# Kernel tuning notes

Measured on AMD Instinct MI355X. Metric: run time of the kernel, lower is better.

Reference implementation:

```python
import jax, jax.numpy as jnp
import numpy as np

EPS = 1e-6
TEMP_GEO = 0.07
W_LOCAL = 0.5
W_SHARP = 0.5


def _l2norm(x):
    return x / jnp.clip(jnp.linalg.norm(x, axis=-1, keepdims=True), 1e-12)


def setup_inputs() -> dict:
    key = jax.random.key(0)
    ks = jax.random.split(key, 6)
    B, L, S, C = 8, 1024, 1024, 128
    N, P = 8, 256
    q_geo = _l2norm(jax.random.normal(ks[0], (B, L, C), jnp.float32))
    geo_pos = _l2norm(jax.random.normal(ks[1], (B, S, C), jnp.float32))
    label = jax.random.randint(ks[2], (B, L, S), 0, 2, jnp.int32)
    q_cl = jax.random.normal(ks[3], (N, P, C), jnp.float32)
    cl_pos = jax.random.normal(ks[4], (N, P, C), jnp.float32)
    idx = jax.random.randint(ks[5], (N,), 0, P, jnp.int32)
    return {"q_geo": q_geo, "q_cl": q_cl, "geo_pos": geo_pos,
            "cl_pos": cl_pos, "label": label, "idx": idx}


def _masked_mean(v, m):
    # per-sample mean over the [L,S] plane of entries where m is True
    m = m.astype(v.dtype)
    return jnp.sum(v * m, axis=(1, 2)) / jnp.maximum(jnp.sum(m, axis=(1, 2)), 1.0)


def _loftr_loss(conf, label):
    # standard LoFTR coarse CE loss (LoFTRLoss source absent from repo snippet)
    conf = jnp.clip(conf, EPS, 1.0 - EPS)
    pos = label == 1
    neg = label == 0
    pos_loss = _masked_mean(-jnp.log(conf), pos)          # [B]
    neg_loss = _masked_mean(-jnp.log(1.0 - conf), neg)    # [B]
    loss = pos_loss + neg_loss
    return jnp.mean(loss), jnp.mean(pos_loss), jnp.mean(neg_loss)


def _geometric_loss(q, k, label):
    sim = jnp.einsum('blc,bsc->bls', q, k) / TEMP_GEO        # [B,L,S]
    conf = jax.nn.softmax(sim, axis=1) * jax.nn.softmax(sim, axis=2)
    return _loftr_loss(conf, label)


def _sharpness_loss(q, k, label):
    sim = (1.0 + jnp.einsum('blc,bsc->bls', q, k)) / 2.0     # [B,L,S]
    # column stats (over L, dim=0 per sample) -> sharpness1 [B,S]
    s1 = (jnp.max(sim, axis=1) - jnp.mean(sim, axis=1)) / jnp.std(sim, axis=1, ddof=1)
    sharp1 = jax.nn.softmax(s1, axis=-1)
    # row stats (over S, dim=1 per sample) -> sharpness2 [B,L]
    s2 = (jnp.max(sim, axis=2) - jnp.mean(sim, axis=2)) / jnp.std(sim, axis=2, ddof=1)
    sharp2 = jax.nn.softmax(s2, axis=-1)
    simc = jnp.clip(sim, EPS, 1.0 - EPS)
    nll = -jnp.log(simc)
    pos = (label == 1).astype(simc.dtype)
    neg = (label == 0)
    loss1 = jnp.sum(nll * sharp1[:, None, :] * pos, axis=(1, 2))   # [B]
    loss2 = jnp.sum(nll * sharp2[:, :, None] * pos, axis=(1, 2))   # [B]
    loss3 = _masked_mean(-jnp.log(1.0 - simc), neg)                # [B]
    losses = (loss1 + loss2) / 2.0 + loss3
    return sharp1, jnp.mean(losses)


def _contrast_loss(q, all_k):
    # intended math of GeCoContrast: full cosine matrix, diag positives, tail negatives
    N = q.shape[0]
    sim = (1.0 + _l2norm(q) @ _l2norm(all_k).T) / 2.0   # [N, M]
    sim = jnp.clip(sim, EPS, 1.0 - EPS)
    l_pos = jnp.diagonal(sim[:, :N])                    # [N]
    l_neg = sim[:, N:]                                  # [N, M-N]
    return (jnp.mean(-jnp.log(l_pos)) + jnp.mean(-jnp.log(1.0 - l_neg))) / 2.0


def _forward(q_geo, q_cl, geo_pos, cl_pos, label, idx):
    loss_geo, geo_pos_loss, geo_neg_loss = _geometric_loss(q_geo, geo_pos, label)
    sharpness, loss_sharp = _sharpness_loss(q_geo, geo_pos, label)
    loss_geo = ((1.0 - W_SHARP) * loss_geo + W_SHARP * loss_sharp) * W_LOCAL

    N, P, C = q_cl.shape
    ar = jnp.arange(N)
    q_sel = q_cl[ar, idx]                               # [N,C]
    sel = cl_pos[ar, idx]                               # [N,C] positives moved to slot 0
    first = cl_pos[:, 0, :]
    swapped = cl_pos.at[ar, idx].set(first).at[:, 0, :].set(sel)
    cl_pos_save = sel
    all_k = jnp.concatenate([swapped[:, 0, :],
                             swapped[:, 1:, :].reshape(N * (P - 1), C)], axis=0)
    loss_cl = _contrast_loss(q_sel, all_k) * (1.0 - W_LOCAL)

    total = loss_geo + loss_cl
    return (sharpness, cl_pos_save, total, geo_pos_loss, geo_neg_loss, loss_sharp, loss_cl)


def reference(q_geo, q_cl, geo_pos, cl_pos, label, idx):
    return _forward(q_geo, q_cl, geo_pos, cl_pos, label, idx)
```

## Files before the change

### kernel.cpp

```cpp
#include <hip/hip_runtime.h>
#include <math.h>

#define BB 8
#define LL 1024
#define SS 1024
#define CC 128
#define NN 8
#define PP 256

static constexpr float EPS       = 1e-6f;
static constexpr float ONE_M_EPS = 1.0f - 1e-6f;
static constexpr float INV_T     = 1.0f / 0.07f;
static constexpr float NLL_MAX   = 13.815511f;
static constexpr float NLL_MIN   = 1.0000005e-6f;

static constexpr size_t DOTSZ      = (size_t)BB * LL * SS;
static constexpr size_t OFF_LSER   = DOTSZ;
static constexpr size_t OFF_LSEC   = DOTSZ + 16384;
static constexpr size_t OFF_SHARP2 = DOTSZ + 32768;
static constexpr size_t OFF_RP     = DOTSZ + 40960;
static constexpr size_t OFF_CP     = OFF_RP + 524288;
static constexpr size_t OFF_ACC    = OFF_CP + 524288;
static constexpr size_t OFF_ACCCL  = OFF_ACC + 48;
static constexpr size_t OFF_QN     = OFF_ACC + 64;

static constexpr int OUT_CLSAVE = 8192;
static constexpr int OUT_SCAL   = 9216;

typedef __bf16 bf16x8 __attribute__((ext_vector_type(8)));
typedef float  floatx4 __attribute__((ext_vector_type(4)));

__device__ __forceinline__ bf16x8 mkfrag(unsigned a, unsigned b, unsigned c, unsigned d) {
    uint4 t = make_uint4(a, b, c, d);
    return __builtin_bit_cast(bf16x8, t);
}

__device__ __forceinline__ void split_f4(float4 x,
                                         unsigned& hp0, unsigned& hp1,
                                         unsigned& lp0, unsigned& lp1) {
    unsigned u0 = __builtin_bit_cast(unsigned, x.x);
    unsigned u1 = __builtin_bit_cast(unsigned, x.y);
    unsigned u2 = __builtin_bit_cast(unsigned, x.z);
    unsigned u3 = __builtin_bit_cast(unsigned, x.w);
    unsigned r0 = u0 + 0x7FFFu + ((u0 >> 16) & 1u);
    unsigned r1 = u1 + 0x7FFFu + ((u1 >> 16) & 1u);
    unsigned r2 = u2 + 0x7FFFu + ((u2 >> 16) & 1u);
    unsigned r3 = u3 + 0x7FFFu + ((u3 >> 16) & 1u);
    float s0 = x.x - __builtin_bit_cast(float, r0 & 0xFFFF0000u);
    float s1 = x.y - __builtin_bit_cast(float, r1 & 0xFFFF0000u);
    float s2 = x.z - __builtin_bit_cast(float, r2 & 0xFFFF0000u);
    float s3 = x.w - __builtin_bit_cast(float, r3 & 0xFFFF0000u);
    hp0 = __builtin_amdgcn_perm(r1, r0, 0x07060302u);
    hp1 = __builtin_amdgcn_perm(r3, r2, 0x07060302u);
    lp0 = __builtin_amdgcn_perm(__builtin_bit_cast(unsigned, s1),
                                __builtin_bit_cast(unsigned, s0), 0x07060302u);
    lp1 = __builtin_amdgcn_perm(__builtin_bit_cast(unsigned, s3),
                                __builtin_bit_cast(unsigned, s2), 0x07060302u);
}

__global__ __launch_bounds__(256) void gemm_dot(const float* __restrict__ A,
                                                const float* __restrict__ Bm,
                                                const float* __restrict__ q_cl,
                                                const float* __restrict__ cl_pos,
                                                const int* __restrict__ idx,
                                                float* __restrict__ out,
                                                float* __restrict__ dot,
                                                float* __restrict__ ws) {
    int tid  = threadIdx.x;
    int lane = tid & 63;
    int w    = tid >> 6;

    if (blockIdx.x == 512) {
        if (tid < 52) ws[OFF_ACC + tid] = 0.0f;
        for (int n = w; n < NN; n += 4) {
            int in = idx[n];
            const float* q = q_cl + ((size_t)(n * PP + in)) * CC;
            float2 qv = *(const float2*)(q + 2 * lane);
            float ss = qv.x * qv.x + qv.y * qv.y;
            for (int o = 32; o; o >>= 1) ss += __shfl_xor(ss, o);
            float inv = 1.0f / fmaxf(sqrtf(ss), 1e-12f);
            *(float2*)(ws + OFF_QN + n * 128 + 2 * lane) = make_float2(qv.x * inv, qv.y * inv);
            const float* cp = cl_pos + ((size_t)(n * PP + in)) * CC;
            float2 cv = *(const float2*)(cp + 2 * lane);
            *(float2*)(out + OUT_CLSAVE + n * 128 + 2 * lane) = cv;
        }
        return;
    }

    int t    = blockIdx.x * 4 + w;
    int b    = t >> 8;
    int rem  = t & 255;
    int lt   = rem >> 4, st = rem & 15;
    int l0   = lt * 64, s0 = st * 64;
    int fl   = lane & 15;
    int quad = lane >> 4;

    const float* Ab = A  + ((size_t)b * LL + l0) * CC;
    const float* Bb = Bm + ((size_t)b * SS + s0) * CC;

    floatx4 acc[4][4];
#pragma unroll
    for (int i = 0; i < 4; i++)
#pragma unroll
        for (int j = 0; j < 4; j++) acc[i][j] = (floatx4){0.f, 0.f, 0.f, 0.f};

    for (int c0 = 0; c0 < 128; c0 += 32) {
        float4 ax[4][2], bx[4][2];
#pragma unroll
        for (int mt = 0; mt < 4; mt++) {
            const float* p = Ab + (size_t)(mt * 16 + fl) * CC + c0 + quad * 8;
            ax[mt][0] = *(const float4*)p;
            ax[mt][1] = *(const float4*)(p + 4);
        }
#pragma unroll
        for (int nt = 0; nt < 4; nt++) {
            const float* p = Bb + (size_t)(nt * 16 + fl) * CC + c0 + quad * 8;
            bx[nt][0] = *(const float4*)p;
            bx[nt][1] = *(const float4*)(p + 4);
        }
        bf16x8 ah[4], al[4];
#pragma unroll
        for (int mt = 0; mt < 4; mt++) {
            unsigned h0, h1, h2, h3, q0, q1, q2, q3;
            split_f4(ax[mt][0], h0, h1, q0, q1);
            split_f4(ax[mt][1], h2, h3, q2, q3);
            ah[mt] = mkfrag(h0, h1, h2, h3);
            al[mt] = mkfrag(q0, q1, q2, q3);
        }
#pragma unroll
        for (int nt = 0; nt < 4; nt++) {
            unsigned h0, h1, h2, h3, q0, q1, q2, q3;
            split_f4(bx[nt][0], h0, h1, q0, q1);
            split_f4(bx[nt][1], h2, h3, q2, q3);
            bf16x8 bh = mkfrag(h0, h1, h2, h3);
            bf16x8 bl = mkfrag(q0, q1, q2, q3);
#pragma unroll
            for (int mt = 0; mt < 4; mt++) {
                acc[mt][nt] = __builtin_amdgcn_mfma_f32_16x16x32_bf16(ah[mt], bh, acc[mt][nt], 0, 0, 0);
                acc[mt][nt] = __builtin_amdgcn_mfma_f32_16x16x32_bf16(ah[mt], bl, acc[mt][nt], 0, 0, 0);
                acc[mt][nt] = __builtin_amdgcn_mfma_f32_16x16x32_bf16(al[mt], bh, acc[mt][nt], 0, 0, 0);
            }
        }
    }

    float* D = dot + ((size_t)b * LL + l0) * SS + s0;
#pragma unroll
    for (int mt = 0; mt < 4; mt++)
#pragma unroll
        for (int nt = 0; nt < 4; nt++) {
            int col = nt * 16 + fl;
#pragma unroll
            for (int r = 0; r < 4; r++) {
                int row = mt * 16 + quad * 4 + r;
                D[(size_t)row * SS + col] = acc[mt][nt][r];
            }
        }

    float ces[4], cmx[4], csm[4], csq[4];
#pragma unroll
    for (int nt = 0; nt < 4; nt++) { ces[nt] = 0.f; cmx[nt] = -1e30f; csm[nt] = 0.f; csq[nt] = 0.f; }
#pragma unroll
    for (int mt = 0; mt < 4; mt++) {
#pragma unroll
        for (int r = 0; r < 4; r++) {
            float es = 0.f, mx = -1e30f, sm = 0.f, sq = 0.f;
#pragma unroll
            for (int nt = 0; nt < 4; nt++) {
                float d  = acc[mt][nt][r];
                float e  = __expf(d * INV_T);
                float s2 = fmaf(0.5f, d, 0.5f);
                es += e; mx = fmaxf(mx, s2); sm += s2; sq += s2 * s2;
                ces[nt] += e; cmx[nt] = fmaxf(cmx[nt], s2); csm[nt] += s2; csq[nt] += s2 * s2;
            }
            for (int o = 1; o < 16; o <<= 1) {
                es += __shfl_xor(es, o);
                mx = fmaxf(mx, __shfl_xor(mx, o));
                sm += __shfl_xor(sm, o);
                sq += __shfl_xor(sq, o);
            }
            if (fl == 0) {
                int row = l0 + mt * 16 + quad * 4 + r;
                *(float4*)(ws + OFF_RP + (((size_t)(b * 16 + st)) * 1024 + row) * 4) =
                    make_float4(es, mx, sm, sq);
            }
        }
    }
#pragma unroll
    for (int nt = 0; nt < 4; nt++) {
        float es = ces[nt], mx = cmx[nt], sm = csm[nt], sq = csq[nt];
        for (int o = 16; o < 64; o <<= 1) {
            es += __shfl_xor(es, o);
            mx = fmaxf(mx, __shfl_xor(mx, o));
            sm += __shfl_xor(sm, o);
            sq += __shfl_xor(sq, o);
        }
        if (quad == 0) {
            int col = s0 + nt * 16 + fl;
            *(float4*)(ws + OFF_CP + (((size_t)(b * 16 + lt)) * 1024 + col) * 4) =
                make_float4(es, mx, sm, sq);
        }
    }
}

__global__ __launch_bounds__(256) void mid(const float* __restrict__ cl_pos,
                                           const int* __restrict__ idx,
                                           float* __restrict__ ws,
                                           float* __restrict__ out) {
    int q   = blockIdx.x;
    int tid = threadIdx.x;
    int lane = tid & 63, wid = tid >> 6;

    if (q < 16) {
        bool docol = (q < 8);
        int b = q & 7;
        const float* part = ws + (docol ? OFF_CP : OFF_RP) + (size_t)b * 16 * 1024 * 4;
        float* lse = ws + (docol ? OFF_LSEC : OFF_LSER) + (size_t)b * 1024;
        float zs[4];
        float mxall = -1e30f;
#pragma unroll
        for (int r = 0; r < 4; r++) {
            int i = tid + r * 256;
            float es = 0.f, mx = -1e30f, sm = 0.f, sq = 0.f;
#pragma unroll
            for (int t = 0; t < 16; t++) {
                float4 v = *(const float4*)(part + ((size_t)t * 1024 + i) * 4);
                es += v.x; mx = fmaxf(mx, v.y); sm += v.z; sq += v.w;
            }
            float mean = sm * (1.0f / 1024.0f);
            float var  = (sq - sm * sm * (1.0f / 1024.0f)) * (1.0f / 1023.0f);
            zs[r] = (mx - mean) / sqrtf(fmaxf(var, 1e-30f));
            mxall = fmaxf(mxall, zs[r]);
            lse[i] = __logf(es);
        }
        __shared__ float sb[4];
        __shared__ float red;
        float mx = mxall;
        for (int o = 32; o; o >>= 1) mx = fmaxf(mx, __shfl_xor(mx, o));
        if (!lane) sb[wid] = mx;
        __syncthreads();
        if (tid == 0) red = fmaxf(fmaxf(sb[0], sb[1]), fmaxf(sb[2], sb[3]));
        __syncthreads();
        mx = red;
        float e[4]; float smv = 0.f;
#pragma unroll
        for (int r = 0; r < 4; r++) { e[r] = __expf(zs[r] - mx); smv += e[r]; }
        for (int o = 32; o; o >>= 1) smv += __shfl_xor(smv, o);
        __syncthreads();
        if (!lane) sb[wid] = smv;
        __syncthreads();
        if (tid == 0) red = sb[0] + sb[1] + sb[2] + sb[3];
        __syncthreads();
        float inv = 1.0f / red;
        float* dst = docol ? (out + (size_t)b * 1024) : (ws + OFF_SHARP2 + (size_t)b * 1024);
#pragma unroll
        for (int r = 0; r < 4; r++) dst[tid + r * 256] = e[r] * inv;
    } else {
        int j = (q - 16) * 4 + wid;
        int m, p;
        if (j < NN) {
            m = j; p = idx[j];
        } else {
            int jj = j - NN;
            m = jj / (PP - 1);
            p = 1 + (jj - m * (PP - 1));
            if (p == idx[m]) p = 0;
        }
        const float* k = cl_pos + ((size_t)(m * PP + p)) * CC;
        float2 kv = *(const float2*)(k + 2 * lane);
        float ksq = kv.x * kv.x + kv.y * kv.y;
        for (int o = 32; o; o >>= 1) ksq += __shfl_xor(ksq, o);
        float invkn = 1.0f / fmaxf(sqrtf(ksq), 1e-12f);
        float pos = 0.0f, neg = 0.0f;
        if (j < NN) {
            const float2 qv = *(const float2*)(ws + OFF_QN + j * 128 + 2 * lane);
            float dt = qv.x * kv.x + qv.y * kv.y;
            for (int o = 32; o; o >>= 1) dt += __shfl_xor(dt, o);
            float sim = fminf(fmaxf(fmaf(0.5f * invkn, dt, 0.5f), EPS), ONE_M_EPS);
            pos = -__logf(sim);
        } else {
#pragma unroll
            for (int n = 0; n < NN; n++) {
                const float2 qv = *(const float2*)(ws + OFF_QN + n * 128 + 2 * lane);
                float dt = qv.x * kv.x + qv.y * kv.y;
                for (int o = 32; o; o >>= 1) dt += __shfl_xor(dt, o);
                float om = fminf(fmaxf(fmaf(-0.5f * invkn, dt, 0.5f), EPS), ONE_M_EPS);
                neg -= __logf(om);
            }
        }
        __shared__ float cb[2][4];
        if (!lane) { cb[0][wid] = pos; cb[1][wid] = neg; }
        __syncthreads();
        if (tid == 0) {
            float ps = cb[0][0] + cb[0][1] + cb[0][2] + cb[0][3];
            float ng = cb[1][0] + cb[1][1] + cb[1][2] + cb[1][3];
            if (ps != 0.0f) atomicAdd(ws + OFF_ACCCL + 0, ps);
            if (ng != 0.0f) atomicAdd(ws + OFF_ACCCL + 1, ng);
        }
    }
}

__device__ __forceinline__ void proc_elem(float d, int lab, float lcj, float sh1j,
                                          float lr, float s2v,
                                          float& posg, float& negg, float& l1, float& l2,
                                          float& negs, float& pcf) {
    float t = lr + lcj - d * (2.0f * INV_T);
    float isPos = (lab == 1) ? 1.0f : 0.0f;
    float isNeg = 1.0f - isPos;
    float tp   = fminf(fmaxf(t, NLL_MIN), NLL_MAX);
    float simc = fminf(fmaxf(fmaf(0.5f, d, 0.5f), EPS), ONE_M_EPS);
    float om   = fminf(fmaxf(fmaf(-0.5f, d, 0.5f), EPS), ONE_M_EPS);
    float nll2 = -__logf(simc);
    float cf   = fminf(fmaxf(__expf(-t), EPS), ONE_M_EPS);
    float nllg = -__logf(1.0f - cf);
    float nlls = -__logf(om);
    posg += isPos * tp;
    l1   += isPos * nll2 * sh1j;
    l2   += isPos * nll2 * s2v;
    pcf  += isPos;
    negg += isNeg * nllg;
    negs += isNeg * nlls;
}

__global__ __launch_bounds__(256) void main_loss(const float* __restrict__ dot,
                                                 const int* __restrict__ label,
                                                 const float* __restrict__ sharp1,
                                                 float* __restrict__ ws) {
    int b = blockIdx.y;
    int l0 = blockIdx.x * 4;
    int s = threadIdx.x * 4;
    float4 lc4 = *(const float4*)(ws + OFF_LSEC + (size_t)b * 1024 + s);
    float4 sh1 = *(const float4*)(sharp1 + (size_t)b * 1024 + s);
    const float* lser = ws + OFF_LSER + (size_t)b * 1024;
    const float* sh2  = ws + OFF_SHARP2 + (size_t)b * 1024;
    float posg = 0, negg = 0, l1 = 0, l2 = 0, negs = 0, pcf = 0;
#pragma unroll
    for (int r = 0; r < 4; r++) {
        int l = l0 + r;
        float lr  = lser[l];
        float s2v = sh2[l];
        size_t base = ((size_t)(b * 1024 + l)) * 1024 + s;
        float4 d4 = *(const float4*)(dot + base);
        int4  lb  = *(const int4*)(label + base);
        proc_elem(d4.x, lb.x, lc4.x, sh1.x, lr, s2v, posg, negg, l1, l2, negs, pcf);
        proc_elem(d4.y, lb.y, lc4.y, sh1.y, lr, s2v, posg, negg, l1, l2, negs, pcf);
        proc_elem(d4.z, lb.z, lc4.z, sh1.z, lr, s2v, posg, negg, l1, l2, negs, pcf);
        proc_elem(d4.w, lb.w, lc4.w, sh1.w, lr, s2v, posg, negg, l1, l2, negs, pcf);
    }
    float vals[6] = {posg, negg, l1, l2, negs, pcf};
    __shared__ float sb[6][4];
    int lane = threadIdx.x & 63, wid = threadIdx.x >> 6;
#pragma unroll
    for (int k = 0; k < 6; k++) {
        float v = vals[k];
        for (int o = 32; o; o >>= 1) v += __shfl_xor(v, o);
        if (!lane) sb[k][wid] = v;
    }
    __syncthreads();
    if (threadIdx.x < 6) {
        float r = sb[threadIdx.x][0] + sb[threadIdx.x][1] + sb[threadIdx.x][2] + sb[threadIdx.x][3];
        atomicAdd(ws + OFF_ACC + (size_t)b * 6 + threadIdx.x, r);
    }
}

__global__ void finalize(float* __restrict__ out, const float* __restrict__ ws) {
    if (threadIdx.x != 0) return;
    float gp = 0, gn = 0, lsh = 0;
    for (int b = 0; b < 8; b++) {
        const float* a = ws + OFF_ACC + (size_t)b * 6;
        float pc = a[5];
        float nc = (float)((size_t)LL * SS) - pc;
        gp += a[0] / fmaxf(pc, 1.0f);
        gn += a[1] / fmaxf(nc, 1.0f);
        lsh += (a[2] + a[3]) * 0.5f + a[4] / fmaxf(nc, 1.0f);
    }
    gp *= 0.125f; gn *= 0.125f; lsh *= 0.125f;
    float lgeo = gp + gn;
    float lgw = (0.5f * lgeo + 0.5f * lsh) * 0.5f;
    float clp = ws[OFF_ACCCL + 0] / 8.0f;
    float cln = ws[OFF_ACCCL + 1] / (8.0f * 2040.0f);
    float lcl = (clp + cln) * 0.5f * 0.5f;
    out[OUT_SCAL + 0] = lgw + lcl;
    out[OUT_SCAL + 1] = gp;
    out[OUT_SCAL + 2] = gn;
    out[OUT_SCAL + 3] = lsh;
    out[OUT_SCAL + 4] = lcl;
}

extern "C" void kernel_launch(void* const* d_in, const int* in_sizes, int n_in,
                              void* d_out, int out_size, void* d_ws, size_t ws_size,
                              hipStream_t stream) {
    const float* q_geo   = (const float*)d_in[0];
    const float* q_cl    = (const float*)d_in[1];
    const float* geo_pos = (const float*)d_in[2];
    const float* cl_pos  = (const float*)d_in[3];
    const int*   label   = (const int*)d_in[4];
    const int*   idx     = (const int*)d_in[5];
    float* out = (float*)d_out;
    float* ws  = (float*)d_ws;
    float* dot = ws;

    gemm_dot<<<dim3(513), dim3(256), 0, stream>>>(q_geo, geo_pos, q_cl, cl_pos, idx, out, dot, ws);
    mid<<<dim3(528), dim3(256), 0, stream>>>(cl_pos, idx, ws, out);
    main_loss<<<dim3(256, 8), dim3(256), 0, stream>>>(dot, label, out, ws);
    finalize<<<dim3(1), dim3(64), 0, stream>>>(out, ws);
}
```

Measured before the change: 158.9 us.

## Recompute similarity GEMM in loss kernel instead of storing dot matrix

Removes the 32 MB fp32 dot-product buffer. The GEMM now runs twice: once to produce row and column statistics, and again in the loss kernel, which consumes the MFMA accumulators directly together with the labels. Tiles shrink to 32x64 per wave to raise block count and cut register use, so column partials grow to 32 slices. This trades extra MFMA work for avoiding a large global write and re-read. Label loads become strided 16-wide per row instead of float4-vectorized.

Result: slower. 201.4 us (+26.7%).

```diff
diff --git a/kernel.cpp b/kernel.cpp
--- a/kernel.cpp
+++ b/kernel.cpp
@@ -14,13 +14,12 @@
 static constexpr float NLL_MAX   = 13.815511f;
 static constexpr float NLL_MIN   = 1.0000005e-6f;
 
-static constexpr size_t DOTSZ      = (size_t)BB * LL * SS;
-static constexpr size_t OFF_LSER   = DOTSZ;
-static constexpr size_t OFF_LSEC   = DOTSZ + 16384;
-static constexpr size_t OFF_SHARP2 = DOTSZ + 32768;
-static constexpr size_t OFF_RP     = DOTSZ + 40960;
+static constexpr size_t OFF_LSER   = 0;
+static constexpr size_t OFF_LSEC   = 8192;
+static constexpr size_t OFF_SHARP2 = 16384;
+static constexpr size_t OFF_RP     = 24576;
 static constexpr size_t OFF_CP     = OFF_RP + 524288;
-static constexpr size_t OFF_ACC    = OFF_CP + 524288;
+static constexpr size_t OFF_ACC    = OFF_CP + 1048576;
 static constexpr size_t OFF_ACCCL  = OFF_ACC + 48;
 static constexpr size_t OFF_QN     = OFF_ACC + 64;
 
@@ -58,19 +57,66 @@
                                 __builtin_bit_cast(unsigned, s2), 0x07060302u);
 }
 
-__global__ __launch_bounds__(256) void gemm_dot(const float* __restrict__ A,
-                                                const float* __restrict__ Bm,
-                                                const float* __restrict__ q_cl,
-                                                const float* __restrict__ cl_pos,
-                                                const int* __restrict__ idx,
-                                                float* __restrict__ out,
-                                                float* __restrict__ dot,
-                                                float* __restrict__ ws) {
+__device__ __forceinline__ void gemm_tile(const float* __restrict__ Ab,
+                                          const float* __restrict__ Bb,
+                                          int fl, int quad, floatx4 acc[2][4]) {
+#pragma unroll
+    for (int i = 0; i < 2; i++)
+#pragma unroll
+        for (int j = 0; j < 4; j++) acc[i][j] = (floatx4){0.f, 0.f, 0.f, 0.f};
+
+    for (int c0 = 0; c0 < 128; c0 += 32) {
+        float4 ax[2][2], bx[4][2];
+#pragma unroll
+        for (int mt = 0; mt < 2; mt++) {
+            const float* p = Ab + (size_t)(mt * 16 + fl) * CC + c0 + quad * 8;
+            ax[mt][0] = *(const float4*)p;
+            ax[mt][1] = *(const float4*)(p + 4);
+        }
+#pragma unroll
+        for (int nt = 0; nt < 4; nt++) {
+            const float* p = Bb + (size_t)(nt * 16 + fl) * CC + c0 + quad * 8;
+            bx[nt][0] = *(const float4*)p;
+            bx[nt][1] = *(const float4*)(p + 4);
+        }
+        bf16x8 ah[2], al[2];
+#pragma unroll
+        for (int mt = 0; mt < 2; mt++) {
+            unsigned h0, h1, h2, h3, q0, q1, q2, q3;
+            split_f4(ax[mt][0], h0, h1, q0, q1);
+            split_f4(ax[mt][1], h2, h3, q2, q3);
+            ah[mt] = mkfrag(h0, h1, h2, h3);
+            al[mt] = mkfrag(q0, q1, q2, q3);
+        }
+#pragma unroll
+        for (int nt = 0; nt < 4; nt++) {
+            unsigned h0, h1, h2, h3, q0, q1, q2, q3;
+            split_f4(bx[nt][0], h0, h1, q0, q1);
+            split_f4(bx[nt][1], h2, h3, q2, q3);
+            bf16x8 bh = mkfrag(h0, h1, h2, h3);
+            bf16x8 bl = mkfrag(q0, q1, q2, q3);
+#pragma unroll
+            for (int mt = 0; mt < 2; mt++) {
+                acc[mt][nt] = __builtin_amdgcn_mfma_f32_16x16x32_bf16(ah[mt], bh, acc[mt][nt], 0, 0, 0);
+                acc[mt][nt] = __builtin_amdgcn_mfma_f32_16x16x32_bf16(ah[mt], bl, acc[mt][nt], 0, 0, 0);
+                acc[mt][nt] = __builtin_amdgcn_mfma_f32_16x16x32_bf16(al[mt], bh, acc[mt][nt], 0, 0, 0);
+            }
+        }
+    }
+}
+
+__global__ __launch_bounds__(256) void gemm_stats(const float* __restrict__ A,
+                                                  const float* __restrict__ Bm,
+                                                  const float* __restrict__ q_cl,
+                                                  const float* __restrict__ cl_pos,
+                                                  const int* __restrict__ idx,
+                                                  float* __restrict__ out,
+                                                  float* __restrict__ ws) {
     int tid  = threadIdx.x;
     int lane = tid & 63;
     int w    = tid >> 6;
 
-    if (blockIdx.x == 512) {
+    if (blockIdx.x == 1024) {
         if (tid < 52) ws[OFF_ACC + tid] = 0.0f;
         for (int n = w; n < NN; n += 4) {
             int in = idx[n];
@@ -88,79 +134,21 @@
     }
 
     int t    = blockIdx.x * 4 + w;
-    int b    = t >> 8;
-    int rem  = t & 255;
+    int b    = t >> 9;
+    int rem  = t & 511;
     int lt   = rem >> 4, st = rem & 15;
-    int l0   = lt * 64, s0 = st * 64;
+    int l0   = lt * 32, s0 = st * 64;
     int fl   = lane & 15;
     int quad = lane >> 4;
 
-    const float* Ab = A  + ((size_t)b * LL + l0) * CC;
-    const float* Bb = Bm + ((size_t)b * SS + s0) * CC;
-
-    floatx4 acc[4][4];
-#pragma unroll
-    for (int i = 0; i < 4; i++)
-#pragma unroll
-        for (int j = 0; j < 4; j++) acc[i][j] = (floatx4){0.f, 0.f, 0.f, 0.f};
-
-    for (int c0 = 0; c0 < 128; c0 += 32) {
-        float4 ax[4][2], bx[4][2];
-#pragma unroll
-        for (int mt = 0; mt < 4; mt++) {
-            const float* p = Ab + (size_t)(mt * 16 + fl) * CC + c0 + quad * 8;
-            ax[mt][0] = *(const float4*)p;
-            ax[mt][1] = *(const float4*)(p + 4);
-        }
-#pragma unroll
-        for (int nt = 0; nt < 4; nt++) {
-            const float* p = Bb + (size_t)(nt * 16 + fl) * CC + c0 + quad * 8;
-            bx[nt][0] = *(const float4*)p;
-            bx[nt][1] = *(const float4*)(p + 4);
-        }
-        bf16x8 ah[4], al[4];
-#pragma unroll
-        for (int mt = 0; mt < 4; mt++) {
-            unsigned h0, h1, h2, h3, q0, q1, q2, q3;
-            split_f4(ax[mt][0], h0, h1, q0, q1);
-            split_f4(ax[mt][1], h2, h3, q2, q3);
-            ah[mt] = mkfrag(h0, h1, h2, h3);
-            al[mt] = mkfrag(q0, q1, q2, q3);
-        }
-#pragma unroll
-        for (int nt = 0; nt < 4; nt++) {
-            unsigned h0, h1, h2, h3, q0, q1, q2, q3;
-            split_f4(bx[nt][0], h0, h1, q0, q1);
-            split_f4(bx[nt][1], h2, h3, q2, q3);
-            bf16x8 bh = mkfrag(h0, h1, h2, h3);
-            bf16x8 bl = mkfrag(q0, q1, q2, q3);
-#pragma unroll
-            for (int mt = 0; mt < 4; mt++) {
-                acc[mt][nt] = __builtin_amdgcn_mfma_f32_16x16x32_bf16(ah[mt], bh, acc[mt][nt], 0, 0, 0);
-                acc[mt][nt] = __builtin_amdgcn_mfma_f32_16x16x32_bf16(ah[mt], bl, acc[mt][nt], 0, 0, 0);
-                acc[mt][nt] = __builtin_amdgcn_mfma_f32_16x16x32_bf16(al[mt], bh, acc[mt][nt], 0, 0, 0);
-            }
-        }
-    }
-
-    float* D = dot + ((size_t)b * LL + l0) * SS + s0;
-#pragma unroll
-    for (int mt = 0; mt < 4; mt++)
-#pragma unroll
-        for (int nt = 0; nt < 4; nt++) {
-            int col = nt * 16 + fl;
-#pragma unroll
-            for (int r = 0; r < 4; r++) {
-                int row = mt * 16 + quad * 4 + r;
-                D[(size_t)row * SS + col] = acc[mt][nt][r];
-            }
-        }
+    floatx4 acc[2][4];
+    gemm_tile(A + ((size_t)b * LL + l0) * CC, Bm + ((size_t)b * SS + s0) * CC, fl, quad, acc);
 
     float ces[4], cmx[4], csm[4], csq[4];
 #pragma unroll
     for (int nt = 0; nt < 4; nt++) { ces[nt] = 0.f; cmx[nt] = -1e30f; csm[nt] = 0.f; csq[nt] = 0.f; }
 #pragma unroll
-    for (int mt = 0; mt < 4; mt++) {
+    for (int mt = 0; mt < 2; mt++) {
 #pragma unroll
         for (int r = 0; r < 4; r++) {
             float es = 0.f, mx = -1e30f, sm = 0.f, sq = 0.f;
@@ -196,7 +184,7 @@
         }
         if (quad == 0) {
             int col = s0 + nt * 16 + fl;
-            *(float4*)(ws + OFF_CP + (((size_t)(b * 16 + lt)) * 1024 + col) * 4) =
+            *(float4*)(ws + OFF_CP + (((size_t)(b * 32 + lt)) * 1024 + col) * 4) =
                 make_float4(es, mx, sm, sq);
         }
     }
@@ -213,7 +201,9 @@
     if (q < 16) {
         bool docol = (q < 8);
         int b = q & 7;
-        const float* part = ws + (docol ? OFF_CP : OFF_RP) + (size_t)b * 16 * 1024 * 4;
+        const float* part = ws + (docol ? (OFF_CP + (size_t)b * 32 * 1024 * 4)
+                                        : (OFF_RP + (size_t)b * 16 * 1024 * 4));
+        int ntile = docol ? 32 : 16;
         float* lse = ws + (docol ? OFF_LSEC : OFF_LSER) + (size_t)b * 1024;
         float zs[4];
         float mxall = -1e30f;
@@ -221,8 +211,7 @@
         for (int r = 0; r < 4; r++) {
             int i = tid + r * 256;
             float es = 0.f, mx = -1e30f, sm = 0.f, sq = 0.f;
-#pragma unroll
-            for (int t = 0; t < 16; t++) {
+            for (int t = 0; t < ntile; t++) {
                 float4 v = *(const float4*)(part + ((size_t)t * 1024 + i) * 4);
                 es += v.x; mx = fmaxf(mx, v.y); sm += v.z; sq += v.w;
             }
@@ -321,44 +310,69 @@
     negs += isNeg * nlls;
 }
 
-__global__ __launch_bounds__(256) void main_loss(const float* __restrict__ dot,
-                                                 const int* __restrict__ label,
-                                                 const float* __restrict__ sharp1,
-                                                 float* __restrict__ ws) {
-    int b = blockIdx.y;
-    int l0 = blockIdx.x * 4;
-    int s = threadIdx.x * 4;
-    float4 lc4 = *(const float4*)(ws + OFF_LSEC + (size_t)b * 1024 + s);
-    float4 sh1 = *(const float4*)(sharp1 + (size_t)b * 1024 + s);
-    const float* lser = ws + OFF_LSER + (size_t)b * 1024;
-    const float* sh2  = ws + OFF_SHARP2 + (size_t)b * 1024;
+__global__ __launch_bounds__(256) void loss_recompute(const float* __restrict__ A,
+                                                      const float* __restrict__ Bm,
+                                                      const int* __restrict__ label,
+                                                      const float* __restrict__ sharp1,
+                                                      float* __restrict__ ws) {
+    int tid  = threadIdx.x;
+    int lane = tid & 63;
+    int w    = tid >> 6;
+    int t    = blockIdx.x * 4 + w;
+    int b    = t >> 9;
+    int rem  = t & 511;
+    int lt   = rem >> 4, st = rem & 15;
+    int l0   = lt * 32, s0 = st * 64;
+    int fl   = lane & 15;
+    int quad = lane >> 4;
+
+    floatx4 acc[2][4];
+    gemm_tile(A + ((size_t)b * LL + l0) * CC, Bm + ((size_t)b * SS + s0) * CC, fl, quad, acc);
+
+    float lrv[2][4], s2v[2][4];
+#pragma unroll
+    for (int mt = 0; mt < 2; mt++)
+#pragma unroll
+        for (int r = 0; r < 4; r++) {
+            int row = l0 + mt * 16 + quad * 4 + r;
+            lrv[mt][r] = ws[OFF_LSER + (size_t)b * 1024 + row];
+            s2v[mt][r] = ws[OFF_SHARP2 + (size_t)b * 1024 + row];
+        }
+    float lcv[4], sh1v[4];
+#pragma unroll
+    for (int nt = 0; nt < 4; nt++) {
+        int col = s0 + nt * 16 + fl;
+        lcv[nt]  = ws[OFF_LSEC + (size_t)b * 1024 + col];
+        sh1v[nt] = sharp1[(size_t)b * 1024 + col];
+    }
+
     float posg = 0, negg = 0, l1 = 0, l2 = 0, negs = 0, pcf = 0;
 #pragma unroll
-    for (int r = 0; r < 4; r++) {
-        int l = l0 + r;
-        float lr  = lser[l];
-        float s2v = sh2[l];
-        size_t base = ((size_t)(b * 1024 + l)) * 1024 + s;
-        float4 d4 = *(const float4*)(dot + base);
-        int4  lb  = *(const int4*)(label + base);
-        proc_elem(d4.x, lb.x, lc4.x, sh1.x, lr, s2v, posg, negg, l1, l2, negs, pcf);
-        proc_elem(d4.y, lb.y, lc4.y, sh1.y, lr, s2v, posg, negg, l1, l2, negs, pcf);
-        proc_elem(d4.z, lb.z, lc4.z, sh1.z, lr, s2v, posg, negg, l1, l2, negs, pcf);
-        proc_elem(d4.w, lb.w, lc4.w, sh1.w, lr, s2v, posg, negg, l1, l2, negs, pcf);
-    }
+    for (int mt = 0; mt < 2; mt++)
+#pragma unroll
+        for (int r = 0; r < 4; r++) {
+            int row = l0 + mt * 16 + quad * 4 + r;
+            const int* lrow = label + ((size_t)(b * 1024 + row)) * 1024 + s0;
+#pragma unroll
+            for (int nt = 0; nt < 4; nt++) {
+                int lab = lrow[nt * 16 + fl];
+                proc_elem(acc[mt][nt][r], lab, lcv[nt], sh1v[nt], lrv[mt][r], s2v[mt][r],
+                          posg, negg, l1, l2, negs, pcf);
+            }
+        }
+
     float vals[6] = {posg, negg, l1, l2, negs, pcf};
     __shared__ float sb[6][4];
-    int lane = threadIdx.x & 63, wid = threadIdx.x >> 6;
 #pragma unroll
     for (int k = 0; k < 6; k++) {
         float v = vals[k];
         for (int o = 32; o; o >>= 1) v += __shfl_xor(v, o);
-        if (!lane) sb[k][wid] = v;
+        if (!lane) sb[k][w] = v;
     }
     __syncthreads();
-    if (threadIdx.x < 6) {
-        float r = sb[threadIdx.x][0] + sb[threadIdx.x][1] + sb[threadIdx.x][2] + sb[threadIdx.x][3];
-        atomicAdd(ws + OFF_ACC + (size_t)b * 6 + threadIdx.x, r);
+    if (tid < 6) {
+        float r = sb[tid][0] + sb[tid][1] + sb[tid][2] + sb[tid][3];
+        atomicAdd(ws + OFF_ACC + (size_t)b * 6 + tid, r);
     }
 }
 
@@ -397,10 +411,9 @@
     const int*   idx     = (const int*)d_in[5];
     float* out = (float*)d_out;
     float* ws  = (float*)d_ws;
-    float* dot = ws;
-
-    gemm_dot<<<dim3(513), dim3(256), 0, stream>>>(q_geo, geo_pos, q_cl, cl_pos, idx, out, dot, ws);
+
+    gemm_stats<<<dim3(1025), dim3(256), 0, stream>>>(q_geo, geo_pos, q_cl, cl_pos, idx, out, ws);
     mid<<<dim3(528), dim3(256), 0, stream>>>(cl_pos, idx, ws, out);
-    main_loss<<<dim3(256, 8), dim3(256), 0, stream>>>(dot, label, out, ws);
+    loss_recompute<<<dim3(1024), dim3(256), 0, stream>>>(q_geo, geo_pos, label, out, ws);
     finalize<<<dim3(1), dim3(64), 0, stream>>>(out, ws);
 }
```

## Stage GEMM tiles through swizzled double-buffered LDS with 128x128 block tiles

Applied to the files above, without the earlier changes.

The dot-product GEMM now has each block cooperatively load a 128x128 output tile's A and B K-slices into XOR-swizzled shared memory. The buffers are double-buffered, with the register prefetch of the next slice overlapping the MFMA work. Before, each wave loaded its own 64x64 operands straight from global memory, so waves in a block did not share operand loads. The goal is less global traffic and latency hidden behind compute, at the cost of LDS use, block barriers and an occupancy hint of 2.

Result: faster. 148.3 us (median of 2 runs) (-6.7%).

```diff
diff --git a/kernel.cpp b/kernel.cpp
--- a/kernel.cpp
+++ b/kernel.cpp
@@ -58,14 +58,30 @@
                                 __builtin_bit_cast(unsigned, s2), 0x07060302u);
 }
 
-__global__ __launch_bounds__(256) void gemm_dot(const float* __restrict__ A,
-                                                const float* __restrict__ Bm,
-                                                const float* __restrict__ q_cl,
-                                                const float* __restrict__ cl_pos,
-                                                const int* __restrict__ idx,
-                                                float* __restrict__ out,
-                                                float* __restrict__ dot,
-                                                float* __restrict__ ws) {
+__device__ __forceinline__ void frag_from_lds(const float* tile, int row, int q,
+                                              bf16x8& hi, bf16x8& lo) {
+    const float* rp = tile + row * 32;
+    int sw = row & 7;
+    float4 x0 = *(const float4*)(rp + (((q * 2)     ^ sw) * 4));
+    float4 x1 = *(const float4*)(rp + (((q * 2 + 1) ^ sw) * 4));
+    unsigned h0, h1, h2, h3, l0, l1, l2, l3;
+    split_f4(x0, h0, h1, l0, l1);
+    split_f4(x1, h2, h3, l2, l3);
+    hi = mkfrag(h0, h1, h2, h3);
+    lo = mkfrag(l0, l1, l2, l3);
+}
+
+__global__ __launch_bounds__(256, 2) void gemm_dot(const float* __restrict__ A,
+                                                   const float* __restrict__ Bm,
+                                                   const float* __restrict__ q_cl,
+                                                   const float* __restrict__ cl_pos,
+                                                   const int* __restrict__ idx,
+                                                   float* __restrict__ out,
+                                                   float* __restrict__ dot,
+                                                   float* __restrict__ ws) {
+    __shared__ __align__(16) float ldsA[2][128 * 32];
+    __shared__ __align__(16) float ldsB[2][128 * 32];
+
     int tid  = threadIdx.x;
     int lane = tid & 63;
     int w    = tid >> 6;
@@ -87,16 +103,27 @@
         return;
     }
 
-    int t    = blockIdx.x * 4 + w;
-    int b    = t >> 8;
-    int rem  = t & 255;
-    int lt   = rem >> 4, st = rem & 15;
-    int l0   = lt * 64, s0 = st * 64;
+    int t  = blockIdx.x;
+    int b  = t >> 6;
+    int rm = t & 63;
+    int bl = rm >> 3, bs = rm & 7;
+    int R0 = bl * 128, C0 = bs * 128;
+
+    const float* Ab = A  + ((size_t)b * LL + R0) * CC;
+    const float* Bb = Bm + ((size_t)b * SS + C0) * CC;
+
+    const float* src  = (w >= 2) ? Bb : Ab;
+    float* dst0 = (w >= 2) ? ldsB[0] : ldsA[0];
+    float* dst1 = (w >= 2) ? ldsB[1] : ldsA[1];
+    int L       = ((w & 1) << 6) | lane;
+    int rowoff  = L >> 3;
+    int chunk   = L & 7;
+    int swz4    = (chunk ^ (rowoff & 7)) * 4;
+
     int fl   = lane & 15;
     int quad = lane >> 4;
-
-    const float* Ab = A  + ((size_t)b * LL + l0) * CC;
-    const float* Bb = Bm + ((size_t)b * SS + s0) * CC;
+    int wr   = w >> 1, wc = w & 1;
+    int Rw   = wr * 64, Cw = wc * 64;
 
     floatx4 acc[4][4];
 #pragma unroll
@@ -104,58 +131,62 @@
 #pragma unroll
         for (int j = 0; j < 4; j++) acc[i][j] = (floatx4){0.f, 0.f, 0.f, 0.f};
 
-    for (int c0 = 0; c0 < 128; c0 += 32) {
-        float4 ax[4][2], bx[4][2];
-#pragma unroll
-        for (int mt = 0; mt < 4; mt++) {
-            const float* p = Ab + (size_t)(mt * 16 + fl) * CC + c0 + quad * 8;
-            ax[mt][0] = *(const float4*)p;
-            ax[mt][1] = *(const float4*)(p + 4);
-        }
+    float4 rg[8];
+#pragma unroll
+    for (int i = 0; i < 8; i++)
+        rg[i] = *(const float4*)(src + (size_t)(i * 16 + rowoff) * CC + chunk * 4);
+#pragma unroll
+    for (int i = 0; i < 8; i++)
+        *(float4*)(dst0 + (i * 16 + rowoff) * 32 + swz4) = rg[i];
+    __syncthreads();
+
+    for (int ks = 0; ks < 4; ks++) {
+        const float* la = (ks & 1) ? ldsA[1] : ldsA[0];
+        const float* lb = (ks & 1) ? ldsB[1] : ldsB[0];
+        float* nxt = ((ks + 1) & 1) ? dst1 : dst0;
+        if (ks < 3) {
+            int k0 = (ks + 1) * 32;
+#pragma unroll
+            for (int i = 0; i < 8; i++)
+                rg[i] = *(const float4*)(src + (size_t)(i * 16 + rowoff) * CC + k0 + chunk * 4);
+        }
+        bf16x8 ah[4], al[4];
+#pragma unroll
+        for (int mt = 0; mt < 4; mt++)
+            frag_from_lds(la, Rw + mt * 16 + fl, quad, ah[mt], al[mt]);
 #pragma unroll
         for (int nt = 0; nt < 4; nt++) {
-            const float* p = Bb + (size_t)(nt * 16 + fl) * CC + c0 + quad * 8;
-            bx[nt][0] = *(const float4*)p;
-            bx[nt][1] = *(const float4*)(p + 4);
-        }
-        bf16x8 ah[4], al[4];
-#pragma unroll
-        for (int mt = 0; mt < 4; mt++) {
-            unsigned h0, h1, h2, h3, q0, q1, q2, q3;
-            split_f4(ax[mt][0], h0, h1, q0, q1);
-            split_f4(ax[mt][1], h2, h3, q2, q3);
-            ah[mt] = mkfrag(h0, h1, h2, h3);
-            al[mt] = mkfrag(q0, q1, q2, q3);
-        }
+            bf16x8 bh, blo;
+            frag_from_lds(lb, Cw + nt * 16 + fl, quad, bh, blo);
+#pragma unroll
+            for (int mt = 0; mt < 4; mt++) {
+                acc[mt][nt] = __builtin_amdgcn_mfma_f32_16x16x32_bf16(ah[mt], bh,  acc[mt][nt], 0, 0, 0);
+                acc[mt][nt] = __builtin_amdgcn_mfma_f32_16x16x32_bf16(ah[mt], blo, acc[mt][nt], 0, 0, 0);
+                acc[mt][nt] = __builtin_amdgcn_mfma_f32_16x16x32_bf16(al[mt], bh,  acc[mt][nt], 0, 0, 0);
+            }
+        }
+        if (ks < 3) {
+#pragma unroll
+            for (int i = 0; i < 8; i++)
+                *(float4*)(nxt + (i * 16 + rowoff) * 32 + swz4) = rg[i];
+        }
+        __syncthreads();
+    }
+
+#pragma unroll
+    for (int mt = 0; mt < 4; mt++)
 #pragma unroll
         for (int nt = 0; nt < 4; nt++) {
-            unsigned h0, h1, h2, h3, q0, q1, q2, q3;
-            split_f4(bx[nt][0], h0, h1, q0, q1);
-            split_f4(bx[nt][1], h2, h3, q2, q3);
-            bf16x8 bh = mkfrag(h0, h1, h2, h3);
-            bf16x8 bl = mkfrag(q0, q1, q2, q3);
-#pragma unroll
-            for (int mt = 0; mt < 4; mt++) {
-                acc[mt][nt] = __builtin_amdgcn_mfma_f32_16x16x32_bf16(ah[mt], bh, acc[mt][nt], 0, 0, 0);
-                acc[mt][nt] = __builtin_amdgcn_mfma_f32_16x16x32_bf16(ah[mt], bl, acc[mt][nt], 0, 0, 0);
-                acc[mt][nt] = __builtin_amdgcn_mfma_f32_16x16x32_bf16(al[mt], bh, acc[mt][nt], 0, 0, 0);
-            }
-        }
-    }
-
-    float* D = dot + ((size_t)b * LL + l0) * SS + s0;
-#pragma unroll
-    for (int mt = 0; mt < 4; mt++)
-#pragma unroll
-        for (int nt = 0; nt < 4; nt++) {
-            int col = nt * 16 + fl;
+            int col = C0 + Cw + nt * 16 + fl;
 #pragma unroll
             for (int r = 0; r < 4; r++) {
-                int row = mt * 16 + quad * 4 + r;
-                D[(size_t)row * SS + col] = acc[mt][nt][r];
-            }
-        }
-
+                int row = R0 + Rw + mt * 16 + quad * 4 + r;
+                dot[((size_t)(b * 1024 + row)) * 1024 + col] = acc[mt][nt][r];
+            }
+        }
+
+    int stile = bs * 2 + wc;
+    int ltile = bl * 2 + wr;
     float ces[4], cmx[4], csm[4], csq[4];
 #pragma unroll
     for (int nt = 0; nt < 4; nt++) { ces[nt] = 0.f; cmx[nt] = -1e30f; csm[nt] = 0.f; csq[nt] = 0.f; }
@@ -179,8 +210,8 @@
                 sq += __shfl_xor(sq, o);
             }
             if (fl == 0) {
-                int row = l0 + mt * 16 + quad * 4 + r;
-                *(float4*)(ws + OFF_RP + (((size_t)(b * 16 + st)) * 1024 + row) * 4) =
+                int row = R0 + Rw + mt * 16 + quad * 4 + r;
+                *(float4*)(ws + OFF_RP + (((size_t)(b * 16 + stile)) * 1024 + row) * 4) =
                     make_float4(es, mx, sm, sq);
             }
         }
@@ -195,8 +226,8 @@
             sq += __shfl_xor(sq, o);
         }
         if (quad == 0) {
-            int col = s0 + nt * 16 + fl;
-            *(float4*)(ws + OFF_CP + (((size_t)(b * 16 + lt)) * 1024 + col) * 4) =
+            int col = C0 + Cw + nt * 16 + fl;
+            *(float4*)(ws + OFF_CP + (((size_t)(b * 16 + ltile)) * 1024 + col) * 4) =
                 make_float4(es, mx, sm, sq);
         }
     }
@@ -213,7 +244,7 @@
     if (q < 16) {
         bool docol = (q < 8);
         int b = q & 7;
-        const float* part = ws + (docol ? OFF_CP : OFF_RP) + (size_t)b * 16 * 1024 * 4;
+        const float* part = ws + (docol ? OFF_CP : OFF_RP);
         float* lse = ws + (docol ? OFF_LSEC : OFF_LSER) + (size_t)b * 1024;
         float zs[4];
         float mxall = -1e30f;
@@ -223,7 +254,7 @@
             float es = 0.f, mx = -1e30f, sm = 0.f, sq = 0.f;
 #pragma unroll
             for (int t = 0; t < 16; t++) {
-                float4 v = *(const float4*)(part + ((size_t)t * 1024 + i) * 4);
+                float4 v = *(const float4*)(part + (((size_t)(b * 16 + t)) * 1024 + i) * 4);
                 es += v.x; mx = fmaxf(mx, v.y); sm += v.z; sq += v.w;
             }
             float mean = sm * (1.0f / 1024.0f);
```
